# Kernel optimization log

Measured on AMD Instinct MI355X. Metric: run time of the kernel, lower is better.

## Reference

```python
import jax, jax.numpy as jnp
import numpy as np

G = 32            # gridsize
N = G * G         # num_nodes = 1024
F_IN = 32         # input_dim
H = 256           # hidden_dim
L = 4             # n_layers
B = 64            # batch
MID = F_IN + L * H
MIN_VAL = -10000000.0
EPS_LN = 1e-5
EPS_BN = 1e-5


def _grid_edges():
    ids = np.arange(N).reshape(G, G)
    hs, hd = ids[:, :-1].ravel(), ids[:, 1:].ravel()
    vs, vd = ids[:-1, :].ravel(), ids[1:, :].ravel()
    src = np.concatenate([hs, hd, vs, vd]).astype(np.int32)
    dst = np.concatenate([hd, hs, vd, vs]).astype(np.int32)
    return jnp.asarray(src), jnp.asarray(dst)


def setup_inputs() -> dict:
    key = jax.random.key(0)
    ks = jax.random.split(key, 16)
    mask_f = jax.random.bernoulli(ks[0], 0.7, (B, N)).astype(jnp.float32)
    feats = jax.random.normal(ks[1], (B, N * F_IN), dtype=jnp.float32)
    observations = jnp.concatenate([mask_f, feats], axis=1)
    src, dst = _grid_edges()
    def lin(k, fi, fo):
        return jax.random.normal(k, (fi, fo), dtype=jnp.float32) / np.sqrt(fi)
    W0 = lin(ks[2], F_IN, H); b0 = jnp.zeros((H,), jnp.float32)
    g0 = jnp.ones((H,), jnp.float32); be0 = jnp.zeros((H,), jnp.float32)
    Ws = jax.random.normal(ks[3], (L - 1, H, H), jnp.float32) / np.sqrt(H)
    bs = jnp.zeros((L - 1, H), jnp.float32)
    gs = jnp.ones((L - 1, H), jnp.float32); bes = jnp.zeros((L - 1, H), jnp.float32)
    W1 = lin(ks[4], MID, 2 * H); b1 = jnp.zeros((2 * H,), jnp.float32)
    bn_g = jnp.ones((2 * H,), jnp.float32); bn_b = jnp.zeros((2 * H,), jnp.float32)
    bn_m = jax.random.normal(ks[5], (2 * H,), jnp.float32) * 0.1
    bn_v = jax.random.uniform(ks[6], (2 * H,), jnp.float32, 0.5, 1.5)
    W2 = lin(ks[7], 2 * H, 1); b2 = jnp.zeros((1,), jnp.float32)
    return {"observations": observations, "src": src, "dst": dst,
            "W0": W0, "b0": b0, "g0": g0, "be0": be0,
            "Ws": Ws, "bs": bs, "gs": gs, "bes": bes,
            "W1": W1, "b1": b1, "bn_g": bn_g, "bn_b": bn_b,
            "bn_m": bn_m, "bn_v": bn_v, "W2": W2, "b2": b2}


def _layer_norm(z, g, b):
    mu = z.mean(-1, keepdims=True)
    var = z.var(-1, keepdims=True)
    return (z - mu) / jnp.sqrt(var + EPS_LN) * g + b


def reference(observations, src, dst, W0, b0, g0, be0, Ws, bs, gs, bes,
              W1, b1, bn_g, bn_b, bn_m, bn_v, W2, b2):
    mask = observations[:, :N] != 0.0                      # [B,N] bool action mask
    x = observations[:, N:].reshape(B, N, F_IN)            # node features
    outs = [x]
    h = x
    for l in range(L):
        # GIN with eps=-1: (1+eps)*x_i vanishes -> mlp(sum of neighbor features)
        agg = jnp.zeros_like(h).at[:, dst, :].add(h[:, src, :])
        W, bb, g, be = ((W0, b0, g0, be0) if l == 0
                        else (Ws[l - 1], bs[l - 1], gs[l - 1], bes[l - 1]))
        h = jax.nn.relu(_layer_norm(agg @ W + bb, g, be))  # mlp ReLU; outer .relu() is idempotent
        outs.append(h)
    xc = jnp.concatenate(outs, axis=-1).reshape(B * N, MID)
    z = xc @ W1 + b1
    z = (z - bn_m) / jnp.sqrt(bn_v + EPS_BN) * bn_g + bn_b  # BatchNorm1d eval mode
    z = jax.nn.relu(z)                                       # dropout off in eval
    y = (z @ W2 + b2).reshape(B, N)
    return jnp.where(mask, y, MIN_VAL)
```

## Files before the change

kernel.cpp:

```cpp
#include <hip/hip_runtime.h>
#include <stdint.h>

#define FIN 32
#define HD 256
#define MIDK 1056
#define HF 512
#define MROWS 65536
#define OBS_STRIDE 33792

typedef float f32x2 __attribute__((ext_vector_type(2)));
typedef float f32x4 __attribute__((ext_vector_type(4)));


__device__ __forceinline__ unsigned pack4fp8(float a, float b, float c, float d) {
    int w = __builtin_amdgcn_cvt_pk_fp8_f32(a, b, 0, false);
    return (unsigned)__builtin_amdgcn_cvt_pk_fp8_f32(c, d, w, true);
}
__device__ __forceinline__ unsigned char f2fp8(float f) {
    return (unsigned char)(__builtin_amdgcn_cvt_pk_fp8_f32(f, f, 0, false) & 0xff);
}

__device__ __forceinline__ void glds16(const void* g, void* l) {
    __builtin_amdgcn_global_load_lds(
        (const __attribute__((address_space(1))) unsigned int*)g,
        (__attribute__((address_space(3))) unsigned int*)l,
        16, 0, 0);
}

__device__ __forceinline__ void gather16(const float* __restrict__ src, int stride, int n,
                                         unsigned char* __restrict__ dst) {
    float f[16];
#pragma unroll
    for (int j = 0; j < 16; ++j) f[j] = src[(size_t)j * stride + n];
    uint4 o;
    o.x = pack4fp8(f[0],  f[1],  f[2],  f[3]);
    o.y = pack4fp8(f[4],  f[5],  f[6],  f[7]);
    o.z = pack4fp8(f[8],  f[9],  f[10], f[11]);
    o.w = pack4fp8(f[12], f[13], f[14], f[15]);
    *(uint4*)dst = o;
}

__global__ __launch_bounds__(256) void k_prep_w(
        const float* __restrict__ W0, const float* __restrict__ Ws,
        const float* __restrict__ W1,
        unsigned char* __restrict__ Wt0, unsigned char* __restrict__ WtL,
        unsigned char* __restrict__ WtF) {
    const int b = blockIdx.x, t = threadIdx.x;
    if (b < 2) {
        int s = b * 256 + t;
        int hh = s >> 8, n = s & 255;
        gather16(W0 + (size_t)(hh * 16) * HD, HD, n, Wt0 + (size_t)s * 16);
    } else if (b < 50) {
        int u = (b - 2) * 256 + t;
        int l = u >> 12, s = u & 4095;
        int kb = s >> 9, hh = (s >> 8) & 1, n = s & 255;
        gather16(Ws + (size_t)l * 65536 + (size_t)(kb * 32 + hh * 16) * HD, HD, n,
                 WtL + (size_t)l * 65536 + (size_t)s * 16);
    } else {
        int s = (b - 50) * 256 + t;
        int kb = s >> 11, hh = (s >> 9) & 3, n = s & 511;
        int k0 = kb * 64 + hh * 16;
        if (k0 < MIDK)
            gather16(W1 + (size_t)k0 * HF, HF, n, WtF + (size_t)s * 16);
        else
            *(uint4*)(WtF + (size_t)s * 16) = make_uint4(0, 0, 0, 0);
    }
}

template <int K>
__global__ __launch_bounds__(256, 4) void k_layer(
        const unsigned char* __restrict__ Hin,
        const float* __restrict__ obs,
        const unsigned char* __restrict__ Wt,
        const float* __restrict__ bias, const float* __restrict__ gamma,
        const float* __restrict__ beta, unsigned char* __restrict__ Hout) {
    constexpr int KB = K / 32;
    __shared__ __align__(16) unsigned char Agg[(K / 16) * 64 * 16];
    __shared__ float ls[64], lss[64];
    const int t = threadIdx.x;
    const int w = t >> 6, lane = t & 63, quad = lane >> 4, l15 = lane & 15;
    const int q1 = quad >> 1, q0 = quad & 1;
    const int m0 = ((blockIdx.x & 7) * 128 + (blockIdx.x >> 3)) * 64;
    const int img = m0 >> 10, node0 = m0 & 1023;
    if (t < 64) { ls[t] = 0.f; lss[t] = 0.f; }

    if constexpr (K == 256) {
        const int r = t & 63, sg = t >> 6;
        const int node = node0 + r;
        const int rr = node >> 5, cc = node & 31;
        const unsigned char* Hb = Hin + (size_t)img * 262144;
#pragma unroll
        for (int p = 0; p < 2; ++p) {
            const int seg = p * 4 + sg;
            float s[32];
#pragma unroll
            for (int i = 0; i < 32; ++i) s[i] = 0.f;
            auto addn = [&](int nn) {
                uint4 u0 = *(const uint4*)(Hb + ((size_t)(2 * seg) * 1024 + nn) * 16);
                uint4 u1 = *(const uint4*)(Hb + ((size_t)(2 * seg + 1) * 1024 + nn) * 16);
                unsigned uu[8] = {u0.x, u0.y, u0.z, u0.w, u1.x, u1.y, u1.z, u1.w};
#pragma unroll
                for (int i = 0; i < 8; ++i) {
                    f32x2 lo = __builtin_amdgcn_cvt_pk_f32_fp8(uu[i], false);
                    f32x2 hi = __builtin_amdgcn_cvt_pk_f32_fp8(uu[i], true);
                    s[4 * i + 0] += lo.x; s[4 * i + 1] += lo.y;
                    s[4 * i + 2] += hi.x; s[4 * i + 3] += hi.y;
                }
            };
            if (cc > 0)  addn(node - 1);
            if (cc < 31) addn(node + 1);
            if (rr > 0)  addn(node - 32);
            if (rr < 31) addn(node + 32);
            unsigned ow[8];
#pragma unroll
            for (int i = 0; i < 8; ++i)
                ow[i] = pack4fp8(s[4 * i], s[4 * i + 1], s[4 * i + 2], s[4 * i + 3]);
            ((uint4*)Agg)[(2 * seg) * 64 + r]     = make_uint4(ow[0], ow[1], ow[2], ow[3]);
            ((uint4*)Agg)[(2 * seg + 1) * 64 + r] = make_uint4(ow[4], ow[5], ow[6], ow[7]);
        }
    } else {
        const int r = t >> 2, seg4 = t & 3;
        const int node = node0 + r;
        const int rr = node >> 5, cc = node & 31;
        const float* fb = obs + (size_t)img * OBS_STRIDE + 1024 + seg4 * 8;
        float s[8] = {0, 0, 0, 0, 0, 0, 0, 0};
        auto addnf = [&](int nn) {
            const float4* fp = (const float4*)(fb + nn * 32);
            float4 f0 = fp[0], f1 = fp[1];
            s[0] += f0.x; s[1] += f0.y; s[2] += f0.z; s[3] += f0.w;
            s[4] += f1.x; s[5] += f1.y; s[6] += f1.z; s[7] += f1.w;
        };
        if (cc > 0)  addnf(node - 1);
        if (cc < 31) addnf(node + 1);
        if (rr > 0)  addnf(node - 32);
        if (rr < 31) addnf(node + 32);
        uint2 o;
        o.x = pack4fp8(s[0], s[1], s[2], s[3]);
        o.y = pack4fp8(s[4], s[5], s[6], s[7]);
        *(uint2*)(Agg + ((seg4 >> 1) * 64 + r) * 16 + (seg4 & 1) * 8) = o;
    }
    __syncthreads();

    f32x4 acc[4][4] = {};
    const unsigned char* bbase = Wt + ((size_t)(q1 * 256 + w * 64 + l15)) * 16 + q0 * 8;
    const unsigned char* abase = Agg + ((size_t)(q1 * 64 + l15)) * 16 + q0 * 8;

#define LOADBL(dst, kb) { const unsigned char* bp = bbase + (size_t)(kb) * 8192; \
    dst[0] = *(const long long*)(bp);        dst[1] = *(const long long*)(bp + 256); \
    dst[2] = *(const long long*)(bp + 512);  dst[3] = *(const long long*)(bp + 768); }
#define MFMAL(buf, kb) { long long af[4]; \
    _Pragma("unroll") for (int mt = 0; mt < 4; ++mt) \
        af[mt] = *(const long long*)(abase + (kb) * 2048 + mt * 256); \
    _Pragma("unroll") for (int mt = 0; mt < 4; ++mt) \
    _Pragma("unroll") for (int nt = 0; nt < 4; ++nt) \
        acc[mt][nt] = __builtin_amdgcn_mfma_f32_16x16x32_fp8_fp8(af[mt], buf[nt], acc[mt][nt], 0, 0, 0); }

    if constexpr (KB == 1) {
        long long bA[4];
        LOADBL(bA, 0);
        MFMAL(bA, 0);
    } else {
        long long bA[4], bB[4];
        LOADBL(bA, 0);
#pragma unroll
        for (int j = 0; j < KB / 2 - 1; ++j) {
            LOADBL(bB, 2 * j + 1);
            MFMAL(bA, 2 * j);
            LOADBL(bA, 2 * j + 2);
            MFMAL(bB, 2 * j + 1);
        }
        LOADBL(bB, KB - 1);
        MFMAL(bA, KB - 2);
        MFMAL(bB, KB - 1);
    }
#undef LOADBL
#undef MFMAL

#pragma unroll
    for (int mt = 0; mt < 4; ++mt) {
        float s0 = 0, s1 = 0, s2 = 0, s3 = 0, u0 = 0, u1 = 0, u2 = 0, u3 = 0;
#pragma unroll
        for (int nt = 0; nt < 4; ++nt) {
            int col = w * 64 + nt * 16 + l15;
            float bv = bias[col];
            f32x4 vv = acc[mt][nt];
            vv.x += bv; vv.y += bv; vv.z += bv; vv.w += bv;
            acc[mt][nt] = vv;
            s0 += vv.x; u0 += vv.x * vv.x;
            s1 += vv.y; u1 += vv.y * vv.y;
            s2 += vv.z; u2 += vv.z * vv.z;
            s3 += vv.w; u3 += vv.w * vv.w;
        }
#pragma unroll
        for (int msk = 1; msk < 16; msk <<= 1) {
            s0 += __shfl_xor(s0, msk); u0 += __shfl_xor(u0, msk);
            s1 += __shfl_xor(s1, msk); u1 += __shfl_xor(u1, msk);
            s2 += __shfl_xor(s2, msk); u2 += __shfl_xor(u2, msk);
            s3 += __shfl_xor(s3, msk); u3 += __shfl_xor(u3, msk);
        }
        if (l15 == 0) {
            int rl = mt * 16 + quad * 4;
            atomicAdd(&ls[rl + 0], s0); atomicAdd(&lss[rl + 0], u0);
            atomicAdd(&ls[rl + 1], s1); atomicAdd(&lss[rl + 1], u1);
            atomicAdd(&ls[rl + 2], s2); atomicAdd(&lss[rl + 2], u2);
            atomicAdd(&ls[rl + 3], s3); atomicAdd(&lss[rl + 3], u3);
        }
    }
    __syncthreads();
#pragma unroll
    for (int mt = 0; mt < 4; ++mt) {
        int rl = mt * 16 + quad * 4;
        float mu0 = ls[rl + 0] * (1.f / 256.f), mu1 = ls[rl + 1] * (1.f / 256.f);
        float mu2 = ls[rl + 2] * (1.f / 256.f), mu3 = ls[rl + 3] * (1.f / 256.f);
        float rs0 = rsqrtf(lss[rl + 0] * (1.f / 256.f) - mu0 * mu0 + 1e-5f);
        float rs1 = rsqrtf(lss[rl + 1] * (1.f / 256.f) - mu1 * mu1 + 1e-5f);
        float rs2 = rsqrtf(lss[rl + 2] * (1.f / 256.f) - mu2 * mu2 + 1e-5f);
        float rs3 = rsqrtf(lss[rl + 3] * (1.f / 256.f) - mu3 * mu3 + 1e-5f);
#pragma unroll
        for (int nt = 0; nt < 4; ++nt) {
            int col = w * 64 + nt * 16 + l15;
            float gg = gamma[col], be = beta[col];
            f32x4 vv = acc[mt][nt];
            size_t rb = ((size_t)(img * 16 + w * 4 + nt) * 1024
                         + node0 + mt * 16 + quad * 4) * 16 + l15;
            Hout[rb]      = f2fp8(fmaxf((vv.x - mu0) * rs0 * gg + be, 0.f));
            Hout[rb + 16] = f2fp8(fmaxf((vv.y - mu1) * rs1 * gg + be, 0.f));
            Hout[rb + 32] = f2fp8(fmaxf((vv.z - mu2) * rs2 * gg + be, 0.f));
            Hout[rb + 48] = f2fp8(fmaxf((vv.w - mu3) * rs3 * gg + be, 0.f));
        }
    }
}

__global__ __launch_bounds__(512) void k_final(
        const unsigned char* __restrict__ h0, const unsigned char* __restrict__ h1,
        const unsigned char* __restrict__ h2, const unsigned char* __restrict__ h3,
        const unsigned char* __restrict__ WtF,
        const float* __restrict__ b1,
        const float* __restrict__ bng, const float* __restrict__ bnb,
        const float* __restrict__ bnm, const float* __restrict__ bnv,
        const float* __restrict__ W2, const float* __restrict__ b2,
        const float* __restrict__ obs, float* __restrict__ out) {
    __shared__ __align__(16) unsigned char As[264 * 16];
    __shared__ __align__(16) unsigned char Bsm[2056 * 16];
    __shared__ float yred[64];
    const int t = threadIdx.x;
    const int w = t >> 6, lane = t & 63, quad = lane >> 4, l15 = lane & 15;
    const int q1 = quad >> 1, q0 = quad & 1;
    const int wr = w >> 2, wc = w & 3;
    const int m0 = ((blockIdx.x & 7) * 128 + (blockIdx.x >> 3)) * 64;
    const int bimg = m0 >> 10, node0 = m0 & 1023;
    if (t < 64) yred[t] = 0.f;

    const unsigned char* hbuf[4] = {h0, h1, h2, h3};
    f32x4 acc[2][8] = {};

    for (int iter = 0; iter < 17; ++iter) {
        const int kb = iter * 64;
        const int steps = (iter < 16) ? 2 : 1;
        if (iter == 0) {
            if (t < 128) {
                int h = t >> 6, r = t & 63;
                const float* p = obs + (size_t)bimg * OBS_STRIDE + 1024 + (node0 + r) * 32 + h * 16;
                float4 f0 = *(const float4*)p, f1 = *(const float4*)(p + 4);
                float4 f2 = *(const float4*)(p + 8), f3 = *(const float4*)(p + 12);
                uint4 o;
                o.x = pack4fp8(f0.x, f0.y, f0.z, f0.w);
                o.y = pack4fp8(f1.x, f1.y, f1.z, f1.w);
                o.z = pack4fp8(f2.x, f2.y, f2.z, f2.w);
                o.w = pack4fp8(f3.x, f3.y, f3.z, f3.w);
                *(uint4*)(As + (h * 66 + r) * 16) = o;
            } else if (t < 256) {
                int h = t >> 6, r = t & 63;
                glds16(h0 + ((size_t)(bimg * 16 + (h - 2)) * 1024 + node0 + r) * 16,
                       As + (size_t)h * 66 * 16);
            }
        } else if (t < steps * 128) {
            int h = t >> 6, r = t & 63;
            int j = kb + h * 16 - FIN;
            glds16(hbuf[j >> 8] + ((size_t)(bimg * 16 + ((j & 255) >> 4)) * 1024 + node0 + r) * 16,
                   As + (size_t)h * 66 * 16);
        }
        for (int i = 0; i < steps * 2; ++i)
            glds16(WtF + ((size_t)iter * 2048 + i * 512 + t) * 16,
                   Bsm + ((size_t)i * 514 + (t & ~63)) * 16);
        __syncthreads();
#pragma unroll 2
        for (int s2 = 0; s2 < steps; ++s2) {
            long long af[2], bf[8];
#pragma unroll
            for (int mt = 0; mt < 2; ++mt)
                af[mt] = *(const long long*)(As + ((s2 * 2 + q1) * 66 + wr * 32 + mt * 16 + l15) * 16 + q0 * 8);
#pragma unroll
            for (int nt = 0; nt < 8; ++nt)
                bf[nt] = *(const long long*)(Bsm + ((size_t)((s2 * 2 + q1) * 514 + wc * 128 + nt * 16 + l15)) * 16 + q0 * 8);
#pragma unroll
            for (int mt = 0; mt < 2; ++mt)
#pragma unroll
                for (int nt = 0; nt < 8; ++nt)
                    acc[mt][nt] = __builtin_amdgcn_mfma_f32_16x16x32_fp8_fp8(af[mt], bf[nt], acc[mt][nt], 0, 0, 0);
        }
        __syncthreads();
    }

    float scv[8], sbv[8], w2v[8];
#pragma unroll
    for (int nt = 0; nt < 8; ++nt) {
        int col = wc * 128 + nt * 16 + l15;
        float sc = bng[col] * rsqrtf(bnv[col] + 1e-5f);
        scv[nt] = sc;
        sbv[nt] = (b1[col] - bnm[col]) * sc + bnb[col];
        w2v[nt] = W2[col];
    }
#pragma unroll
    for (int mt = 0; mt < 2; ++mt) {
        float p0 = 0, p1 = 0, p2 = 0, p3 = 0;
#pragma unroll
        for (int nt = 0; nt < 8; ++nt) {
            f32x4 vv = acc[mt][nt];
            p0 += fmaxf(vv.x * scv[nt] + sbv[nt], 0.f) * w2v[nt];
            p1 += fmaxf(vv.y * scv[nt] + sbv[nt], 0.f) * w2v[nt];
            p2 += fmaxf(vv.z * scv[nt] + sbv[nt], 0.f) * w2v[nt];
            p3 += fmaxf(vv.w * scv[nt] + sbv[nt], 0.f) * w2v[nt];
        }
#pragma unroll
        for (int msk = 1; msk < 16; msk <<= 1) {
            p0 += __shfl_xor(p0, msk);
            p1 += __shfl_xor(p1, msk);
            p2 += __shfl_xor(p2, msk);
            p3 += __shfl_xor(p3, msk);
        }
        if (l15 == 0) {
            int rl = wr * 32 + mt * 16 + quad * 4;
            atomicAdd(&yred[rl + 0], p0);
            atomicAdd(&yred[rl + 1], p1);
            atomicAdd(&yred[rl + 2], p2);
            atomicAdd(&yred[rl + 3], p3);
        }
    }
    __syncthreads();
    if (t < 64) {
        int gm = m0 + t;
        float mk = obs[(size_t)bimg * OBS_STRIDE + (node0 + t)];
        out[gm] = (mk != 0.f) ? yred[t] + b2[0] : -10000000.0f;
    }
}

extern "C" void kernel_launch(void* const* d_in, const int* in_sizes, int n_in,
                              void* d_out, int out_size, void* d_ws, size_t ws_size,
                              hipStream_t stream) {
    const float* obs = (const float*)d_in[0];
    const float* W0  = (const float*)d_in[3];
    const float* b0  = (const float*)d_in[4];
    const float* g0  = (const float*)d_in[5];
    const float* be0 = (const float*)d_in[6];
    const float* Ws  = (const float*)d_in[7];
    const float* bs  = (const float*)d_in[8];
    const float* gs  = (const float*)d_in[9];
    const float* bes = (const float*)d_in[10];
    const float* W1  = (const float*)d_in[11];
    const float* b1  = (const float*)d_in[12];
    const float* bng = (const float*)d_in[13];
    const float* bnb = (const float*)d_in[14];
    const float* bnm = (const float*)d_in[15];
    const float* bnv = (const float*)d_in[16];
    const float* W2  = (const float*)d_in[17];
    const float* b2  = (const float*)d_in[18];
    float* out = (float*)d_out;

    char* ws = (char*)d_ws;
    unsigned char* h0  = (unsigned char*)(ws);
    unsigned char* h1  = (unsigned char*)(ws + 16777216);
    unsigned char* h2  = (unsigned char*)(ws + 33554432);
    unsigned char* h3  = (unsigned char*)(ws + 50331648);
    unsigned char* Wt0 = (unsigned char*)(ws + 67108864);
    unsigned char* WtL = (unsigned char*)(ws + 67117056);
    unsigned char* WtF = (unsigned char*)(ws + 67313664);

    k_prep_w<<<182, 256, 0, stream>>>(W0, Ws, W1, Wt0, WtL, WtF);

    k_layer<FIN><<<1024, 256, 0, stream>>>(h0 , obs, Wt0, b0, g0, be0, h0);
    k_layer<HD> <<<1024, 256, 0, stream>>>(h0, obs, WtL,              bs,       gs,       bes,       h1);
    k_layer<HD> <<<1024, 256, 0, stream>>>(h1, obs, WtL + 65536,      bs + 256, gs + 256, bes + 256, h2);
    k_layer<HD> <<<1024, 256, 0, stream>>>(h2, obs, WtL + 2 * 65536,  bs + 512, gs + 512, bes + 512, h3);

    k_final<<<1024, 512, 0, stream>>>(h0, h1, h2, h3, WtF, b1, bng, bnb, bnm, bnv,
                                      W2, b2, obs, out);
}
```

Before: 235.7 us.

## Double-buffer final GEMM LDS tiles with async prefetch and manual waitcnt

```diff
diff --git a/kernel.cpp b/kernel.cpp
--- a/kernel.cpp
+++ b/kernel.cpp
@@ -25,6 +25,14 @@
         (const __attribute__((address_space(1))) unsigned int*)g,
         (__attribute__((address_space(3))) unsigned int*)l,
         16, 0, 0);
+}
+
+#define WAITV(N) asm volatile("s_waitcnt vmcnt(" #N ")" ::: "memory")
+#define WAITLGKM0() asm volatile("s_waitcnt lgkmcnt(0)" ::: "memory")
+__device__ __forceinline__ void barx() {
+    asm volatile("" ::: "memory");
+    __builtin_amdgcn_s_barrier();
+    asm volatile("" ::: "memory");
 }
 
 __device__ __forceinline__ void gather16(const float* __restrict__ src, int stride, int n,
@@ -240,8 +248,8 @@
         const float* __restrict__ bnm, const float* __restrict__ bnv,
         const float* __restrict__ W2, const float* __restrict__ b2,
         const float* __restrict__ obs, float* __restrict__ out) {
-    __shared__ __align__(16) unsigned char As[264 * 16];
-    __shared__ __align__(16) unsigned char Bsm[2056 * 16];
+    __shared__ __align__(16) unsigned char As[2][264 * 16];
+    __shared__ __align__(16) unsigned char Bsm[2][2056 * 16];
     __shared__ float yred[64];
     const int t = threadIdx.x;
     const int w = t >> 6, lane = t & 63, quad = lane >> 4, l15 = lane & 15;
@@ -254,52 +262,81 @@
     const unsigned char* hbuf[4] = {h0, h1, h2, h3};
     f32x4 acc[2][8] = {};
 
-    for (int iter = 0; iter < 17; ++iter) {
-        const int kb = iter * 64;
-        const int steps = (iter < 16) ? 2 : 1;
-        if (iter == 0) {
-            if (t < 128) {
-                int h = t >> 6, r = t & 63;
-                const float* p = obs + (size_t)bimg * OBS_STRIDE + 1024 + (node0 + r) * 32 + h * 16;
-                float4 f0 = *(const float4*)p, f1 = *(const float4*)(p + 4);
-                float4 f2 = *(const float4*)(p + 8), f3 = *(const float4*)(p + 12);
-                uint4 o;
-                o.x = pack4fp8(f0.x, f0.y, f0.z, f0.w);
-                o.y = pack4fp8(f1.x, f1.y, f1.z, f1.w);
-                o.z = pack4fp8(f2.x, f2.y, f2.z, f2.w);
-                o.w = pack4fp8(f3.x, f3.y, f3.z, f3.w);
-                *(uint4*)(As + (h * 66 + r) * 16) = o;
-            } else if (t < 256) {
-                int h = t >> 6, r = t & 63;
-                glds16(h0 + ((size_t)(bimg * 16 + (h - 2)) * 1024 + node0 + r) * 16,
-                       As + (size_t)h * 66 * 16);
-            }
-        } else if (t < steps * 128) {
+    auto stageB = [&](int it, unsigned char* Bb, int nB) {
+#pragma unroll
+        for (int i = 0; i < nB; ++i)
+            glds16(WtF + ((size_t)it * 2048 + (size_t)i * 512 + t) * 16,
+                   Bb + ((size_t)i * 514 + (t & ~63)) * 16);
+    };
+    auto stageA = [&](int it, unsigned char* Ab, int steps) {
+        if (t < steps * 128) {
             int h = t >> 6, r = t & 63;
-            int j = kb + h * 16 - FIN;
+            int j = it * 64 + h * 16 - FIN;
             glds16(hbuf[j >> 8] + ((size_t)(bimg * 16 + ((j & 255) >> 4)) * 1024 + node0 + r) * 16,
-                   As + (size_t)h * 66 * 16);
-        }
-        for (int i = 0; i < steps * 2; ++i)
-            glds16(WtF + ((size_t)iter * 2048 + i * 512 + t) * 16,
-                   Bsm + ((size_t)i * 514 + (t & ~63)) * 16);
-        __syncthreads();
-#pragma unroll 2
+                   Ab + (size_t)h * 66 * 16);
+        }
+    };
+    auto compute = [&](const unsigned char* Ab, const unsigned char* Bb, int steps) {
         for (int s2 = 0; s2 < steps; ++s2) {
             long long af[2], bf[8];
 #pragma unroll
             for (int mt = 0; mt < 2; ++mt)
-                af[mt] = *(const long long*)(As + ((s2 * 2 + q1) * 66 + wr * 32 + mt * 16 + l15) * 16 + q0 * 8);
+                af[mt] = *(const long long*)(Ab + ((s2 * 2 + q1) * 66 + wr * 32 + mt * 16 + l15) * 16 + q0 * 8);
 #pragma unroll
             for (int nt = 0; nt < 8; ++nt)
-                bf[nt] = *(const long long*)(Bsm + ((size_t)((s2 * 2 + q1) * 514 + wc * 128 + nt * 16 + l15)) * 16 + q0 * 8);
+                bf[nt] = *(const long long*)(Bb + ((size_t)((s2 * 2 + q1) * 514 + wc * 128 + nt * 16 + l15)) * 16 + q0 * 8);
+            __builtin_amdgcn_s_setprio(1);
 #pragma unroll
             for (int mt = 0; mt < 2; ++mt)
 #pragma unroll
                 for (int nt = 0; nt < 8; ++nt)
                     acc[mt][nt] = __builtin_amdgcn_mfma_f32_16x16x32_fp8_fp8(af[mt], bf[nt], acc[mt][nt], 0, 0, 0);
-        }
-        __syncthreads();
+            __builtin_amdgcn_s_setprio(0);
+        }
+    };
+
+    if (t < 128) {
+        int h = t >> 6, r = t & 63;
+        const float* p = obs + (size_t)bimg * OBS_STRIDE + 1024 + (node0 + r) * 32 + h * 16;
+        float4 f0 = *(const float4*)p, f1 = *(const float4*)(p + 4);
+        float4 f2 = *(const float4*)(p + 8), f3 = *(const float4*)(p + 12);
+        uint4 o;
+        o.x = pack4fp8(f0.x, f0.y, f0.z, f0.w);
+        o.y = pack4fp8(f1.x, f1.y, f1.z, f1.w);
+        o.z = pack4fp8(f2.x, f2.y, f2.z, f2.w);
+        o.w = pack4fp8(f3.x, f3.y, f3.z, f3.w);
+        *(uint4*)(As[0] + (h * 66 + r) * 16) = o;
+    } else if (t < 256) {
+        int h = t >> 6, r = t & 63;
+        glds16(h0 + ((size_t)(bimg * 16 + (h - 2)) * 1024 + node0 + r) * 16,
+               As[0] + (size_t)h * 66 * 16);
+    }
+    stageB(0, Bsm[0], 4);
+    stageA(1, As[1], 2);
+    stageB(1, Bsm[1], 4);
+    if (w < 4) { WAITV(5); } else { WAITV(4); }
+    WAITLGKM0();
+    barx();
+    compute(As[0], Bsm[0], 2);
+    barx();
+
+#pragma unroll 1
+    for (int it = 1; it < 17; ++it) {
+        const int cur = it & 1;
+        if (it < 15) {
+            stageA(it + 1, As[cur ^ 1], 2);
+            stageB(it + 1, Bsm[cur ^ 1], 4);
+            if (w < 4) { WAITV(5); } else { WAITV(4); }
+        } else if (it == 15) {
+            stageA(16, As[cur ^ 1], 1);
+            stageB(16, Bsm[cur ^ 1], 2);
+            if (w < 2) { WAITV(3); } else { WAITV(2); }
+        } else {
+            WAITV(0);
+        }
+        barx();
+        compute(As[cur], Bsm[cur], (it < 16) ? 2 : 1);
+        barx();
     }
 
     float scv[8], sbv[8], w2v[8];
```

New measurement: 234.3 us. No clear change (-0.6%).
